# Optimization experiments

Measured on AMD Instinct MI355X. Metric: run time of the kernel, lower is better.

The kernel has to match this reference:

```python
import jax, jax.numpy as jnp
import numpy as np

ALPHA_LINK = 2.0  # alpha_link from __init__


def setup_inputs() -> dict:
    key = jax.random.key(0)
    B, C = 65536, 1000
    k0, k1, k2, k3 = jax.random.split(key, 4)
    y_pred = jax.random.normal(k0, (B, C), dtype=jnp.float32)
    y_true = jax.random.randint(k1, (B,), 0, C)
    weight = jax.random.uniform(k2, (C,), dtype=jnp.float32)
    # dense boolean class-link matrix: link_matrix[gt, pred] == True means pred is linked to gt
    link_matrix = jax.random.randint(k3, (C, C), 0, 2).astype(jnp.bool_)
    return {"y_pred": y_pred, "y_true": y_true, "weight": weight, "link_matrix": link_matrix}


def reference(y_pred, y_true, weight, link_matrix):
    # per-sample penalty: alpha_link if (pred != gt) and pred is linked to gt, else 1
    pred = jnp.argmax(y_pred, axis=1)                      # [B]
    linked = link_matrix[y_true, pred]                     # [B] bool gather
    penalty = jnp.where((pred != y_true) & linked, ALPHA_LINK, 1.0)  # [B]

    # weighted cross-entropy, reduction='none' semantics: loss_i = weight[y_i] * nll_i
    logp = jax.nn.log_softmax(y_pred, axis=1)              # [B, C]
    nll = -jnp.take_along_axis(logp, y_true[:, None], axis=1)[:, 0]  # [B]
    ce = weight[y_true] * nll                              # [B]

    return jnp.mean(penalty * ce)
```

## Files before the change

kernel.cpp:

```cpp
#include <hip/hip_runtime.h>
#include <math.h>


#define B_SAMPLES 65536
#define C_CLASSES 1000
#define C4 250

__global__ __launch_bounds__(256) void lce_kernel(
    const float* __restrict__ y_pred,
    const int* __restrict__ y_true,
    const float* __restrict__ weight,
    const int* __restrict__ link,
    float* __restrict__ out)
{
    const int lane = threadIdx.x & 63;
    const int wave = threadIdx.x >> 6;
    const int gwave = blockIdx.x * 4 + wave;
    const int nwaves = gridDim.x * 4;

    float local = 0.0f;

    for (int s = gwave; s < B_SAMPLES; s += nwaves) {
        const float4* row = (const float4*)(y_pred + (size_t)s * C_CLASSES);

        float4 v[4];
        #pragma unroll
        for (int it = 0; it < 4; ++it) {
            int idx = it * 64 + lane;
            if (idx < C4) {
                v[it] = row[idx];
            } else {
                v[it] = make_float4(-INFINITY, -INFINITY, -INFINITY, -INFINITY);
            }
        }

        float m = -INFINITY;
        int am = 0;
        #pragma unroll
        for (int it = 0; it < 4; ++it) {
            const float* p = (const float*)&v[it];
            #pragma unroll
            for (int j = 0; j < 4; ++j) {
                float x = p[j];
                int col = (it * 64 + lane) * 4 + j;
                if (x > m) { m = x; am = col; }
            }
        }

        float sum = 0.0f;
        #pragma unroll
        for (int it = 0; it < 4; ++it) {
            const float* p = (const float*)&v[it];
            #pragma unroll
            for (int j = 0; j < 4; ++j) {
                sum += __expf(p[j] - m);
            }
        }

        #pragma unroll
        for (int off = 32; off > 0; off >>= 1) {
            float om  = __shfl_xor(m, off, 64);
            float os  = __shfl_xor(sum, off, 64);
            int   oam = __shfl_xor(am, off, 64);
            float M = fmaxf(m, om);
            sum = sum * __expf(m - M) + os * __expf(om - M);
            am = (om > m || (om == m && oam < am)) ? oam : am;
            m = M;
        }

        if (lane == 0) {
            int t = y_true[s];
            float xt = y_pred[(size_t)s * C_CLASSES + t];
            float nll = m + __logf(sum) - xt;
            float pen = (am != t && link[(size_t)t * C_CLASSES + am] != 0)
                            ? 2.0f : 1.0f;
            local += pen * weight[t] * nll;
        }
    }

    __shared__ float wsum[4];
    if (lane == 0) wsum[wave] = local;
    __syncthreads();
    if (threadIdx.x == 0) {
        float total = (wsum[0] + wsum[1] + wsum[2] + wsum[3]) * (1.0f / B_SAMPLES);
        atomicAdd(out, total);
    }
}

extern "C" void kernel_launch(void* const* d_in, const int* in_sizes, int n_in,
                              void* d_out, int out_size, void* d_ws, size_t ws_size,
                              hipStream_t stream) {
    const float* y_pred = (const float*)d_in[0];
    const int* y_true   = (const int*)d_in[1];
    const float* weight = (const float*)d_in[2];
    const int* link     = (const int*)d_in[3];
    float* out          = (float*)d_out;

    hipMemsetAsync(out, 0, sizeof(float), stream);

    lce_kernel<<<2048, 256, 0, stream>>>(y_pred, y_true, weight, link, out);
}
```

Baseline: 365.2 us.

## Double-buffer row loads with nontemporal reads and extract target logit via shuffle

After: 356.7 us. 2.3% less time.

```diff
diff --git a/kernel.cpp b/kernel.cpp
--- a/kernel.cpp
+++ b/kernel.cpp
@@ -5,6 +5,26 @@
 #define B_SAMPLES 65536
 #define C_CLASSES 1000
 #define C4 250
+#define NBLOCKS 2048
+#define NWAVES (NBLOCKS * 4)
+#define SPW (B_SAMPLES / NWAVES)
+
+typedef float f4 __attribute__((ext_vector_type(4)));
+
+__device__ __forceinline__ void load_row_nt(f4* dst, const float* __restrict__ y_pred,
+                                            int s, int lane)
+{
+    const f4* row = (const f4*)(y_pred + (size_t)s * C_CLASSES);
+    #pragma unroll
+    for (int it = 0; it < 4; ++it) {
+        int idx = it * 64 + lane;
+        if (idx < C4) {
+            dst[it] = __builtin_nontemporal_load(row + idx);
+        } else {
+            dst[it] = (f4){-INFINITY, -INFINITY, -INFINITY, -INFINITY};
+        }
+    }
+}
 
 __global__ __launch_bounds__(256) void lce_kernel(
     const float* __restrict__ y_pred,
@@ -16,44 +36,58 @@
     const int lane = threadIdx.x & 63;
     const int wave = threadIdx.x >> 6;
     const int gwave = blockIdx.x * 4 + wave;
-    const int nwaves = gridDim.x * 4;
 
     float local = 0.0f;
 
-    for (int s = gwave; s < B_SAMPLES; s += nwaves) {
-        const float4* row = (const float4*)(y_pred + (size_t)s * C_CLASSES);
+    f4 va[4], vb[4];
 
-        float4 v[4];
-        #pragma unroll
-        for (int it = 0; it < 4; ++it) {
-            int idx = it * 64 + lane;
-            if (idx < C4) {
-                v[it] = row[idx];
-            } else {
-                v[it] = make_float4(-INFINITY, -INFINITY, -INFINITY, -INFINITY);
-            }
+    load_row_nt(va, y_pred, gwave, lane);
+    int t_cur = y_true[gwave];
+
+    #pragma unroll
+    for (int k = 0; k < SPW; ++k) {
+        const int s = gwave + k * NWAVES;
+
+        int t_next = 0;
+        if (k + 1 < SPW) {
+            f4* dst = (k & 1) ? va : vb;
+            load_row_nt(dst, y_pred, s + NWAVES, lane);
+            t_next = y_true[s + NWAVES];
         }
+        const f4* v = (k & 1) ? vb : va;
+        const int t = t_cur;
 
         float m = -INFINITY;
         int am = 0;
         #pragma unroll
         for (int it = 0; it < 4; ++it) {
-            const float* p = (const float*)&v[it];
             #pragma unroll
             for (int j = 0; j < 4; ++j) {
-                float x = p[j];
+                float x = v[it][j];
                 int col = (it * 64 + lane) * 4 + j;
                 if (x > m) { m = x; am = col; }
+            }
+        }
+
+        const int ct   = t >> 2;
+        const int ln_t = ct & 63;
+        const int it_t = ct >> 6;
+        const int j_t  = t & 3;
+        float xt_part = 0.0f;
+        #pragma unroll
+        for (int it = 0; it < 4; ++it) {
+            #pragma unroll
+            for (int j = 0; j < 4; ++j) {
+                xt_part = (it == it_t && j == j_t) ? v[it][j] : xt_part;
             }
         }
 
         float sum = 0.0f;
         #pragma unroll
         for (int it = 0; it < 4; ++it) {
-            const float* p = (const float*)&v[it];
             #pragma unroll
             for (int j = 0; j < 4; ++j) {
-                sum += __expf(p[j] - m);
+                sum += __expf(v[it][j] - m);
             }
         }
 
@@ -68,14 +102,16 @@
             m = M;
         }
 
+        float xt = __shfl(xt_part, ln_t, 64);
+
         if (lane == 0) {
-            int t = y_true[s];
-            float xt = y_pred[(size_t)s * C_CLASSES + t];
             float nll = m + __logf(sum) - xt;
             float pen = (am != t && link[(size_t)t * C_CLASSES + am] != 0)
                             ? 2.0f : 1.0f;
             local += pen * weight[t] * nll;
         }
+
+        t_cur = t_next;
     }
 
     __shared__ float wsum[4];
@@ -98,5 +134,5 @@
 
     hipMemsetAsync(out, 0, sizeof(float), stream);
 
-    lce_kernel<<<2048, 256, 0, stream>>>(y_pred, y_true, weight, link, out);
+    lce_kernel<<<NBLOCKS, 256, 0, stream>>>(y_pred, y_true, weight, link, out);
 }
```
